# Optimization experiments

Hardware: AMD Instinct MI355X
Metric: run time of the kernel (lower is better)

Reference implementation:

```python
import jax, jax.numpy as jnp
import numpy as np

VOCAB, EMBED, HIDDEN, NCLASS = 50000, 256, 256, 5
B, T = 64, 512


def _lstm_cell(x, h, c, W, U, b):
    # Keras LSTMCell: gate order i, f, g(candidate), o
    z = x @ W + h @ U + b  # [B, 4H]
    i, f, g, o = jnp.split(z, 4, axis=-1)
    i = jax.nn.sigmoid(i)
    f = jax.nn.sigmoid(f)
    g = jnp.tanh(g)
    o = jax.nn.sigmoid(o)
    c_new = f * c + i * g
    h_new = o * jnp.tanh(c_new)
    return h_new, c_new


def _run_stacked(xs, W1, U1, b1, W2, U2, b2):
    # xs: [T, B, E] -> outputs of layer 2: [T, B, H]
    Bb = xs.shape[1]
    H = U1.shape[0]
    zero = jnp.zeros((Bb, H), dtype=xs.dtype)
    init = (zero, zero, zero, zero)

    def step(carry, x_t):
        h1, c1, h2, c2 = carry
        h1, c1 = _lstm_cell(x_t, h1, c1, W1, U1, b1)
        h2, c2 = _lstm_cell(h1, h2, c2, W2, U2, b2)
        return (h1, c1, h2, c2), h2

    _, ys = jax.lax.scan(step, init, xs)
    return ys


def setup_inputs() -> dict:
    key = jax.random.key(0)
    ks = jax.random.split(key, 16)
    s = 0.05

    def mk(k, shape):
        return (jax.random.normal(k, shape, dtype=jnp.float32) * s)

    inp = {
        "tokens": jax.random.randint(ks[0], (B, T), 0, VOCAB, dtype=jnp.int64),
        "embed_table": mk(ks[1], (VOCAB, EMBED)),
        # forward direction, layer 1 and 2
        "fw_W1": mk(ks[2], (EMBED, 4 * HIDDEN)),
        "fw_U1": mk(ks[3], (HIDDEN, 4 * HIDDEN)),
        "fw_b1": jnp.zeros((4 * HIDDEN,), jnp.float32),
        "fw_W2": mk(ks[4], (HIDDEN, 4 * HIDDEN)),
        "fw_U2": mk(ks[5], (HIDDEN, 4 * HIDDEN)),
        "fw_b2": jnp.zeros((4 * HIDDEN,), jnp.float32),
        # backward direction, layer 1 and 2
        "bw_W1": mk(ks[6], (EMBED, 4 * HIDDEN)),
        "bw_U1": mk(ks[7], (HIDDEN, 4 * HIDDEN)),
        "bw_b1": jnp.zeros((4 * HIDDEN,), jnp.float32),
        "bw_W2": mk(ks[8], (HIDDEN, 4 * HIDDEN)),
        "bw_U2": mk(ks[9], (HIDDEN, 4 * HIDDEN)),
        "bw_b2": jnp.zeros((4 * HIDDEN,), jnp.float32),
        # output dense (2H -> 5), softmax
        "dense_W": mk(ks[10], (2 * HIDDEN, NCLASS)),
        "dense_b": jnp.zeros((NCLASS,), jnp.float32),
    }
    return inp


def reference(tokens, embed_table,
              fw_W1, fw_U1, fw_b1, fw_W2, fw_U2, fw_b2,
              bw_W1, bw_U1, bw_b1, bw_W2, bw_U2, bw_b2,
              dense_W, dense_b):
    emb = embed_table[tokens]                    # [B, T, E]
    xs = jnp.swapaxes(emb, 0, 1)                 # [T, B, E]

    ys_fw = _run_stacked(xs, fw_W1, fw_U1, fw_b1, fw_W2, fw_U2, fw_b2)          # [T,B,H]
    ys_bw = _run_stacked(xs[::-1], bw_W1, bw_U1, bw_b1, bw_W2, bw_U2, bw_b2)[::-1]

    feat = jnp.concatenate([ys_fw, ys_bw], axis=-1)   # [T, B, 2H]
    feat = jnp.swapaxes(feat, 0, 1)                   # [B, T, 2H]
    logits = feat @ dense_W + dense_b                 # [B, T, 5]
    return jax.nn.softmax(logits, axis=-1)
```

## Files before the change

### kernel.cpp

```cpp
#include <hip/hip_runtime.h>

typedef __bf16 bf16;
typedef __bf16 bf16x8 __attribute__((ext_vector_type(8)));
typedef float f32x4 __attribute__((ext_vector_type(4)));
typedef unsigned long long u64;

#define T_LEN 512
#define BATCH 64
#define HID 256
#define LDA 520
#define ZLD 67

#define CTRL_BYTES 4096
#define LOG_OFF CTRL_BYTES
#define LOG_BYTES (T_LEN * BATCH * 16 * 5 * 4)
#define RING_OFF (LOG_OFF + LOG_BYTES)
#define HSLOT_U64 4096
#define RING_SLOTS 16
#define RING_U64 (RING_SLOTS * HSLOT_U64)
#define RING_BYTES (4 * RING_U64 * 8)

#define SMEM_A 66560
#define SMEM_Z 17408
#define SMEM_C 4096
#define SMEM_TAIL 576
#define SMEM_BYTES (SMEM_A + SMEM_Z + SMEM_C + SMEM_TAIL)

__device__ inline uint4 cvt8(const float4* s) {
    float4 a = s[0], b = s[1];
    union { uint4 u; bf16 h[8]; } r;
    r.h[0] = (bf16)a.x; r.h[1] = (bf16)a.y; r.h[2] = (bf16)a.z; r.h[3] = (bf16)a.w;
    r.h[4] = (bf16)b.x; r.h[5] = (bf16)b.y; r.h[6] = (bf16)b.z; r.h[7] = (bf16)b.w;
    return r.u;
}

__device__ __forceinline__ void load16(const u64* src, int tid, u64* dst) {
#pragma unroll
    for (int k = 0; k < 16; ++k)
        dst[k] = __hip_atomic_load(src + k * 256 + tid, __ATOMIC_RELAXED, __HIP_MEMORY_SCOPE_SYSTEM);
}

__device__ __forceinline__ void resolve16(const u64* src, int tid, unsigned ep,
                                          unsigned mask, u64* dst) {
    for (;;) {
        unsigned fail = 0u;
#pragma unroll
        for (int k = 0; k < 16; ++k) {
            bool bad = (((mask >> k) & 1u) != 0u) && ((((unsigned)dst[k]) & 1u) != ep);
            if (__any(bad)) fail |= (1u << k);
        }
        if (!fail) break;
        __builtin_amdgcn_s_sleep(2);
#pragma unroll
        for (int k = 0; k < 16; ++k)
            if ((fail >> k) & 1u)
                dst[k] = __hip_atomic_load(src + k * 256 + tid, __ATOMIC_RELAXED, __HIP_MEMORY_SCOPE_SYSTEM);
    }
}

__global__ void __launch_bounds__(256, 1)
lstm_kernel(const int* __restrict__ tokens,
            const float* __restrict__ embed,
            const float* __restrict__ W1f, const float* __restrict__ U1f, const float* __restrict__ b1f,
            const float* __restrict__ W2f, const float* __restrict__ U2f, const float* __restrict__ b2f,
            const float* __restrict__ W1b, const float* __restrict__ U1b, const float* __restrict__ b1b,
            const float* __restrict__ W2b, const float* __restrict__ U2b, const float* __restrict__ b2b,
            const float* __restrict__ dW,
            char* __restrict__ ws)
{
    extern __shared__ char smem[];
    bf16*  Abuf  = (bf16*)smem;
    float* zLds  = (float*)(smem + SMEM_A);
    float* cLds  = (float*)(smem + SMEM_A + SMEM_Z);
    float* bLds  = (float*)(smem + SMEM_A + SMEM_Z + SMEM_C);
    float* dwLds = bLds + 64;

    const int tid = threadIdx.x;
    const int wg  = blockIdx.x;
    const int dir = wg & 1, layer = (wg >> 1) & 1, sub = wg >> 2;

    const float *Wp, *Up, *bp;
    if (dir == 0) { if (layer == 0) { Wp=W1f; Up=U1f; bp=b1f; } else { Wp=W2f; Up=U2f; bp=b2f; } }
    else          { if (layer == 0) { Wp=W1b; Up=U1b; bp=b1b; } else { Wp=W2b; Up=U2b; bp=b2b; } }

    {
        for (int it = 0; it < 32; ++it) {
            int idx = it * 256 + tid;
            int k = idx >> 4, q4 = idx & 15;
            int g = q4 >> 2, u0 = (q4 & 3) * 4;
            const float* src = (k < 256) ? (Wp + (size_t)k * 1024 + g * 256 + sub * 16 + u0)
                                         : (Up + (size_t)(k - 256) * 1024 + g * 256 + sub * 16 + u0);
            float4 v = *(const float4*)src;
            int c0 = g * 16 + u0;
            Abuf[(c0 + 0) * LDA + k] = (bf16)v.x;
            Abuf[(c0 + 1) * LDA + k] = (bf16)v.y;
            Abuf[(c0 + 2) * LDA + k] = (bf16)v.z;
            Abuf[(c0 + 3) * LDA + k] = (bf16)v.w;
        }
        if (tid < 64) {
            int g = tid >> 4, u = tid & 15;
            bLds[tid] = bp[g * 256 + sub * 16 + u];
        }
        if (tid < 80) {
            int u = tid / 5, c = tid % 5;
            dwLds[tid] = dW[(size_t)(dir * 256 + sub * 16 + u) * 5 + c];
        }
        for (int i = tid; i < 1024; i += 256) cLds[i] = 0.f;
    }
    __syncthreads();

    const int wave = tid >> 6, lane = tid & 63, quad = lane >> 4, ln = lane & 15;
    const int mrow0 = (wave >> 1) * 32, ncol0 = (wave & 1) * 32;
    bf16x8 bfrag[2][16];
#pragma unroll
    for (int nt = 0; nt < 2; ++nt)
#pragma unroll
        for (int kt = 0; kt < 16; ++kt)
            bfrag[nt][kt] = *(const bf16x8*)&Abuf[(ncol0 + nt * 16 + ln) * LDA + kt * 32 + quad * 8];
    __syncthreads();

    u64* ringL1  = (u64*)(ws + RING_OFF) + (size_t)(dir * 2 + 0) * RING_U64;
    u64* ringL2  = (u64*)(ws + RING_OFF) + (size_t)(dir * 2 + 1) * RING_U64;
    u64* ringOwn = (layer == 0) ? ringL1 : ringL2;
    float* logits  = (float*)(ws + LOG_OFF);
    unsigned* prog = (unsigned*)ws + dir * 32;

    const int bA = tid >> 2, qA = tid & 3;
    const unsigned ownMask = 0xFFFFu ^ (1u << sub);
    unsigned progCache = 0u;
    u64 pkPrevW = 0ull;

    float4 pf[16];
    int tokB = 0;
    if (layer == 0) {
        const int tt0 = dir ? (T_LEN - 1) : 0;
        int tokA = tokens[bA * T_LEN + tt0];
        const float4* src = (const float4*)(embed + (size_t)tokA * HID + qA * 64);
#pragma unroll
        for (int j = 0; j < 16; ++j) pf[j] = src[j];
        const int tt1 = dir ? (T_LEN - 2) : 1;
        tokB = tokens[bA * T_LEN + tt1];
    }

    for (int s = 0; s < T_LEN; ++s) {
        u64 hreg[16], xreg[16];
        const u64* ownSrc = ringOwn + (size_t)(s & 15) * HSLOT_U64;
        const u64* xSrc   = ringL1 + (size_t)((s + 1) & 15) * HSLOT_U64;
        if (s > 0) load16(ownSrc, tid, hreg);
        if (layer == 1) load16(xSrc, tid, xreg);

        if (layer == 0 && tid == 0 && s >= 13) {
            unsigned need = (unsigned)(s - 12);
            while (progCache < need)
                progCache = __hip_atomic_load(prog, __ATOMIC_RELAXED, __HIP_MEMORY_SCOPE_SYSTEM);
        }

        if (s > 0) {
            resolve16(ownSrc, tid, (unsigned)(((s - 1) >> 4) & 1), ownMask, hreg);
        } else {
#pragma unroll
            for (int k = 0; k < 16; ++k) hreg[k] = 0ull;
        }
        hreg[sub] = pkPrevW;

        if (layer == 0) {
            uint4* dstx = (uint4*)&Abuf[bA * LDA + qA * 64];
#pragma unroll
            for (int j = 0; j < 8; ++j) dstx[j] = cvt8(&pf[2 * j]);
        } else {
            resolve16(xSrc, tid, (unsigned)((s >> 4) & 1), 0xFFFFu, xreg);
#pragma unroll
            for (int k = 0; k < 16; ++k)
                *(u64*)&Abuf[bA * LDA + k * 16 + qA * 4] = xreg[k];
        }
#pragma unroll
        for (int k = 0; k < 16; ++k)
            *(u64*)&Abuf[bA * LDA + 256 + k * 16 + qA * 4] = hreg[k];
        __syncthreads();

        if (layer == 0) {
            const float4* src = (const float4*)(embed + (size_t)tokB * HID + qA * 64);
#pragma unroll
            for (int j = 0; j < 16; ++j) pf[j] = src[j];
            const int sn2 = (s + 2 < T_LEN) ? s + 2 : T_LEN - 1;
            const int tt2 = dir ? (T_LEN - 1 - sn2) : sn2;
            tokB = tokens[bA * T_LEN + tt2];
        }

        f32x4 acc[2][2];
#pragma unroll
        for (int mi = 0; mi < 2; ++mi)
#pragma unroll
            for (int ni = 0; ni < 2; ++ni) acc[mi][ni] = (f32x4)(0.0f);
#pragma unroll
        for (int kt = 0; kt < 16; ++kt) {
            bf16x8 a0 = *(const bf16x8*)&Abuf[(mrow0 + ln) * LDA + kt * 32 + quad * 8];
            bf16x8 a1 = *(const bf16x8*)&Abuf[(mrow0 + 16 + ln) * LDA + kt * 32 + quad * 8];
            acc[0][0] = __builtin_amdgcn_mfma_f32_16x16x32_bf16(a0, bfrag[0][kt], acc[0][0], 0, 0, 0);
            acc[0][1] = __builtin_amdgcn_mfma_f32_16x16x32_bf16(a0, bfrag[1][kt], acc[0][1], 0, 0, 0);
            acc[1][0] = __builtin_amdgcn_mfma_f32_16x16x32_bf16(a1, bfrag[0][kt], acc[1][0], 0, 0, 0);
            acc[1][1] = __builtin_amdgcn_mfma_f32_16x16x32_bf16(a1, bfrag[1][kt], acc[1][1], 0, 0, 0);
        }
#pragma unroll
        for (int mi = 0; mi < 2; ++mi)
#pragma unroll
            for (int ni = 0; ni < 2; ++ni) {
                int row = mrow0 + mi * 16 + quad * 4;
                int col = ncol0 + ni * 16 + ln;
#pragma unroll
                for (int r = 0; r < 4; ++r)
                    zLds[(row + r) * ZLD + col] = acc[mi][ni][r];
            }
        __syncthreads();

        u64* hdst = ringOwn + (size_t)((s + 1) & 15) * HSLOT_U64;
        float hv[4];
        {
            const int b = bA, u0 = qA * 4;
#pragma unroll
            for (int e = 0; e < 4; ++e) {
                int u = u0 + e;
                float zi = zLds[b * ZLD + u]      + bLds[u];
                float zf = zLds[b * ZLD + 16 + u] + bLds[16 + u];
                float zg = zLds[b * ZLD + 32 + u] + bLds[32 + u];
                float zo = zLds[b * ZLD + 48 + u] + bLds[48 + u];
                float ig = 1.f / (1.f + __expf(-zi));
                float fg = 1.f / (1.f + __expf(-zf));
                float gg = 1.f - 2.f / (__expf(2.f * zg) + 1.f);
                float og = 1.f / (1.f + __expf(-zo));
                float cn = fg * cLds[b * 16 + u] + ig * gg;
                cLds[b * 16 + u] = cn;
                hv[e] = og * (1.f - 2.f / (__expf(2.f * cn) + 1.f));
            }
            union { u64 w; bf16 h[4]; } pk;
#pragma unroll
            for (int e = 0; e < 4; ++e) pk.h[e] = (bf16)hv[e];
            pk.w = (pk.w & ~1ull) | (u64)((s >> 4) & 1);
            pkPrevW = pk.w;
            __hip_atomic_store(hdst + sub * 256 + tid, pk.w,
                               __ATOMIC_RELAXED, __HIP_MEMORY_SCOPE_SYSTEM);
        }
        float pr[5];
        if (layer == 1) {
#pragma unroll
            for (int c = 0; c < 5; ++c)
                pr[c] = hv[0] * dwLds[(qA * 4 + 0) * 5 + c] + hv[1] * dwLds[(qA * 4 + 1) * 5 + c]
                      + hv[2] * dwLds[(qA * 4 + 2) * 5 + c] + hv[3] * dwLds[(qA * 4 + 3) * 5 + c];
#pragma unroll
            for (int m = 1; m < 4; m <<= 1)
#pragma unroll
                for (int c = 0; c < 5; ++c) pr[c] += __shfl_xor(pr[c], m);
        }

        if (layer == 1 && tid == 0)
            __hip_atomic_store(prog, (unsigned)(s + 1),
                               __ATOMIC_RELAXED, __HIP_MEMORY_SCOPE_SYSTEM);

        if (layer == 1 && qA == 0) {
            const int tp = dir ? (T_LEN - 1 - s) : s;
            float* lp = &logits[(((size_t)tp * BATCH + bA) * 16 + sub) * 5];
#pragma unroll
            for (int c = 0; c < 5; ++c) lp[c] = pr[c];
        }
    }
}

__global__ void __launch_bounds__(256)
softmax_kernel(const char* __restrict__ ws, const float* __restrict__ dB, float* __restrict__ out)
{
    const int gid = blockIdx.x * 256 + threadIdx.x;
    const int b = gid & 63, t = gid >> 6;
    const float* lp = (const float*)(ws + LOG_OFF) + ((size_t)t * BATCH + b) * 80;
    float l[5];
#pragma unroll
    for (int c = 0; c < 5; ++c) l[c] = dB[c];
#pragma unroll
    for (int sub = 0; sub < 16; ++sub)
#pragma unroll
        for (int c = 0; c < 5; ++c) l[c] += lp[sub * 5 + c];
    float m = l[0];
#pragma unroll
    for (int c = 1; c < 5; ++c) m = fmaxf(m, l[c]);
    float e[5], ssum = 0.f;
#pragma unroll
    for (int c = 0; c < 5; ++c) { e[c] = __expf(l[c] - m); ssum += e[c]; }
    float inv = 1.f / ssum;
    float* o = out + ((size_t)b * T_LEN + t) * 5;
#pragma unroll
    for (int c = 0; c < 5; ++c) o[c] = e[c] * inv;
}

extern "C" void kernel_launch(void* const* d_in, const int* in_sizes, int n_in,
                              void* d_out, int out_size, void* d_ws, size_t ws_size,
                              hipStream_t stream)
{
    const int*   tokens = (const int*)d_in[0];
    const float* embed  = (const float*)d_in[1];
    const float* W1f = (const float*)d_in[2],  *U1f = (const float*)d_in[3],  *b1f = (const float*)d_in[4];
    const float* W2f = (const float*)d_in[5],  *U2f = (const float*)d_in[6],  *b2f = (const float*)d_in[7];
    const float* W1b = (const float*)d_in[8],  *U1b = (const float*)d_in[9],  *b1b = (const float*)d_in[10];
    const float* W2b = (const float*)d_in[11], *U2b = (const float*)d_in[12], *b2b = (const float*)d_in[13];
    const float* dW  = (const float*)d_in[14], *dB  = (const float*)d_in[15];

    hipFuncSetAttribute(reinterpret_cast<const void*>(lstm_kernel),
                        hipFuncAttributeMaxDynamicSharedMemorySize, SMEM_BYTES);
    hipMemsetAsync(d_ws, 0, CTRL_BYTES, stream);
    hipMemsetAsync((char*)d_ws + RING_OFF, 0xFF, RING_BYTES, stream);
    lstm_kernel<<<dim3(64), dim3(256), SMEM_BYTES, stream>>>(
        tokens, embed, W1f, U1f, b1f, W2f, U2f, b2f,
        W1b, U1b, b1b, W2b, U2b, b2b, dW, (char*)d_ws);
    softmax_kernel<<<dim3(128), dim3(256), 0, stream>>>((const char*)d_ws, dB, (float*)d_out);
}
```

Baseline: 3.141 ms.

## Poll per-wave canary flags instead of re-reading full hidden-state ring slots

Adds a small canary array where each wave publishes an epoch bit after its hidden-state stores drain (s_waitcnt vmcnt(0)). Consumers spin on the 16 canary words instead of repeatedly re-reading 16 full ring chunks, and only reload the ring data once the matching canary flips. All atomics drop from system to agent scope, which cuts coherence cost for the cross-block handoff. The risk is ordering: relaxed stores plus vmcnt may not guarantee data visibility before the canary, and the extra store and wait add latency to every step.

```diff
diff --git a/kernel.cpp b/kernel.cpp
--- a/kernel.cpp
+++ b/kernel.cpp
@@ -11,8 +11,10 @@
 #define LDA 520
 #define ZLD 67
 
-#define CTRL_BYTES 4096
-#define LOG_OFF CTRL_BYTES
+#define PROG_BYTES 4096
+#define CAN_OFF PROG_BYTES
+#define CAN_BYTES (4 * 16 * 4 * 16 * 4)
+#define LOG_OFF (CAN_OFF + CAN_BYTES)
 #define LOG_BYTES (T_LEN * BATCH * 16 * 5 * 4)
 #define RING_OFF (LOG_OFF + LOG_BYTES)
 #define HSLOT_U64 4096
@@ -37,24 +39,37 @@
 __device__ __forceinline__ void load16(const u64* src, int tid, u64* dst) {
 #pragma unroll
     for (int k = 0; k < 16; ++k)
-        dst[k] = __hip_atomic_load(src + k * 256 + tid, __ATOMIC_RELAXED, __HIP_MEMORY_SCOPE_SYSTEM);
-}
-
-__device__ __forceinline__ void resolve16(const u64* src, int tid, unsigned ep,
+        dst[k] = __hip_atomic_load(src + k * 256 + tid, __ATOMIC_RELAXED, __HIP_MEMORY_SCOPE_AGENT);
+}
+
+__device__ __forceinline__ void resolve16(const u64* src, const unsigned* canChunk,
+                                          int tid, int lane, unsigned ep,
                                           unsigned mask, u64* dst) {
-    for (;;) {
-        unsigned fail = 0u;
-#pragma unroll
-        for (int k = 0; k < 16; ++k) {
-            bool bad = (((mask >> k) & 1u) != 0u) && ((((unsigned)dst[k]) & 1u) != ep);
-            if (__any(bad)) fail |= (1u << k);
-        }
-        if (!fail) break;
-        __builtin_amdgcn_s_sleep(2);
+    unsigned fail = 0u;
+#pragma unroll
+    for (int k = 0; k < 16; ++k) {
+        bool bad = (((mask >> k) & 1u) != 0u) && ((((unsigned)dst[k]) & 1u) != ep);
+        if (__any(bad)) fail |= (1u << k);
+    }
+    const int cl = lane & 15;
+    while (fail) {
+        for (;;) {
+            unsigned cv = __hip_atomic_load(canChunk + cl, __ATOMIC_RELAXED, __HIP_MEMORY_SCOPE_AGENT);
+            bool pend = (((fail >> cl) & 1u) != 0u) && ((cv & 1u) != ep);
+            if (!__any(pend)) break;
+            __builtin_amdgcn_s_sleep(1);
+        }
 #pragma unroll
         for (int k = 0; k < 16; ++k)
             if ((fail >> k) & 1u)
-                dst[k] = __hip_atomic_load(src + k * 256 + tid, __ATOMIC_RELAXED, __HIP_MEMORY_SCOPE_SYSTEM);
+                dst[k] = __hip_atomic_load(src + k * 256 + tid, __ATOMIC_RELAXED, __HIP_MEMORY_SCOPE_AGENT);
+        unsigned nf = 0u;
+#pragma unroll
+        for (int k = 0; k < 16; ++k) {
+            bool bad = (((fail >> k) & 1u) != 0u) && ((((unsigned)dst[k]) & 1u) != ep);
+            if (__any(bad)) nf |= (1u << k);
+        }
+        fail = nf;
     }
 }
 
@@ -122,6 +137,9 @@
     u64* ringL1  = (u64*)(ws + RING_OFF) + (size_t)(dir * 2 + 0) * RING_U64;
     u64* ringL2  = (u64*)(ws + RING_OFF) + (size_t)(dir * 2 + 1) * RING_U64;
     u64* ringOwn = (layer == 0) ? ringL1 : ringL2;
+    unsigned* canAll    = (unsigned*)(ws + CAN_OFF);
+    unsigned* canOwnRng = canAll + (size_t)(dir * 2 + layer) * 16 * 4 * 16;
+    unsigned* canL1Rng  = canAll + (size_t)(dir * 2 + 0) * 16 * 4 * 16;
     float* logits  = (float*)(ws + LOG_OFF);
     unsigned* prog = (unsigned*)ws + dir * 32;
 
@@ -152,11 +170,12 @@
         if (layer == 0 && tid == 0 && s >= 13) {
             unsigned need = (unsigned)(s - 12);
             while (progCache < need)
-                progCache = __hip_atomic_load(prog, __ATOMIC_RELAXED, __HIP_MEMORY_SCOPE_SYSTEM);
+                progCache = __hip_atomic_load(prog, __ATOMIC_RELAXED, __HIP_MEMORY_SCOPE_AGENT);
         }
 
         if (s > 0) {
-            resolve16(ownSrc, tid, (unsigned)(((s - 1) >> 4) & 1), ownMask, hreg);
+            resolve16(ownSrc, canOwnRng + (s & 15) * 64 + wave * 16,
+                      tid, lane, (unsigned)(((s - 1) >> 4) & 1), ownMask, hreg);
         } else {
 #pragma unroll
             for (int k = 0; k < 16; ++k) hreg[k] = 0ull;
@@ -168,7 +187,8 @@
 #pragma unroll
             for (int j = 0; j < 8; ++j) dstx[j] = cvt8(&pf[2 * j]);
         } else {
-            resolve16(xSrc, tid, (unsigned)((s >> 4) & 1), 0xFFFFu, xreg);
+            resolve16(xSrc, canL1Rng + ((s + 1) & 15) * 64 + wave * 16,
+                      tid, lane, (unsigned)((s >> 4) & 1), 0xFFFFu, xreg);
 #pragma unroll
             for (int k = 0; k < 16; ++k)
                 *(u64*)&Abuf[bA * LDA + k * 16 + qA * 4] = xreg[k];
@@ -238,7 +258,7 @@
             pk.w = (pk.w & ~1ull) | (u64)((s >> 4) & 1);
             pkPrevW = pk.w;
             __hip_atomic_store(hdst + sub * 256 + tid, pk.w,
-                               __ATOMIC_RELAXED, __HIP_MEMORY_SCOPE_SYSTEM);
+                               __ATOMIC_RELAXED, __HIP_MEMORY_SCOPE_AGENT);
         }
         float pr[5];
         if (layer == 1) {
@@ -252,16 +272,22 @@
                 for (int c = 0; c < 5; ++c) pr[c] += __shfl_xor(pr[c], m);
         }
 
-        if (layer == 1 && tid == 0)
-            __hip_atomic_store(prog, (unsigned)(s + 1),
-                               __ATOMIC_RELAXED, __HIP_MEMORY_SCOPE_SYSTEM);
-
         if (layer == 1 && qA == 0) {
             const int tp = dir ? (T_LEN - 1 - s) : s;
             float* lp = &logits[(((size_t)tp * BATCH + bA) * 16 + sub) * 5];
 #pragma unroll
             for (int c = 0; c < 5; ++c) lp[c] = pr[c];
         }
+
+        if (layer == 1 && tid == 0)
+            __hip_atomic_store(prog, (unsigned)(s + 1),
+                               __ATOMIC_RELAXED, __HIP_MEMORY_SCOPE_AGENT);
+
+        asm volatile("s_waitcnt vmcnt(0)" ::: "memory");
+        if (lane == 0)
+            __hip_atomic_store(canOwnRng + ((s + 1) & 15) * 64 + wave * 16 + sub,
+                               (unsigned)((s >> 4) & 1),
+                               __ATOMIC_RELAXED, __HIP_MEMORY_SCOPE_AGENT);
     }
 }
 
@@ -304,7 +330,8 @@
 
     hipFuncSetAttribute(reinterpret_cast<const void*>(lstm_kernel),
                         hipFuncAttributeMaxDynamicSharedMemorySize, SMEM_BYTES);
-    hipMemsetAsync(d_ws, 0, CTRL_BYTES, stream);
+    hipMemsetAsync(d_ws, 0, PROG_BYTES, stream);
+    hipMemsetAsync((char*)d_ws + CAN_OFF, 0xFF, CAN_BYTES, stream);
     hipMemsetAsync((char*)d_ws + RING_OFF, 0xFF, RING_BYTES, stream);
     lstm_kernel<<<dim3(64), dim3(256), SMEM_BYTES, stream>>>(
         tokens, embed, W1f, U1f, b1f, W2f, U2f, b2f,
```

After: 3.093 ms. No clear change (-1.5%).
